# Optimization experiments

Measured on AMD Instinct MI355X. Metric: run time of the kernel, lower is better.

## Reference

```python
import jax, jax.numpy as jnp
import numpy as np


def _rotate_nearest(img, theta):
    """Rotate a batch of images (B, C, H, W) counterclockwise by theta radians
    about the image center, nearest-neighbor sampling, zero fill outside
    (matches torchvision rotate defaults: InterpolationMode.NEAREST, expand=False)."""
    B, C, H, W = img.shape
    cy = (H - 1) / 2.0
    cx = (W - 1) / 2.0
    ys = jnp.arange(H, dtype=jnp.float32) - cy
    xs = jnp.arange(W, dtype=jnp.float32) - cx
    yg, xg = jnp.meshgrid(ys, xs, indexing="ij")  # (H, W)
    c = jnp.cos(theta)
    s = jnp.sin(theta)
    # inverse affine map: output pixel -> source pixel
    x_src = c * xg + s * yg + cx
    y_src = -s * xg + c * yg + cy
    xi = jnp.round(x_src).astype(jnp.int32)
    yi = jnp.round(y_src).astype(jnp.int32)
    valid = (xi >= 0) & (xi < W) & (yi >= 0) & (yi < H)
    xi = jnp.clip(xi, 0, W - 1)
    yi = jnp.clip(yi, 0, H - 1)
    out = img[:, :, yi, xi]  # gather -> (B, C, H, W)
    return jnp.where(valid, out, jnp.zeros((), img.dtype))


def reference(image, kernel_size):
    # image: (B, C, H, W, A); A = num_angles
    B, C, H, W, A = image.shape
    angle_increment = 360.0 / A
    offsets = (jnp.arange(A) % kernel_size).astype(jnp.float32)
    # torch code calls rotate(slice, -angle_increment * relative_offset) in degrees
    thetas = jnp.deg2rad(-angle_increment * offsets)  # (A,)
    img_a = jnp.moveaxis(image, -1, 0)  # (A, B, C, H, W)
    rot = jax.vmap(_rotate_nearest, in_axes=(0, 0))(img_a, thetas)  # (A, B, C, H, W)
    rot = jnp.moveaxis(rot, 0, -1)  # (B, C, H, W, A)
    # MaxPool3d(kernel=(1,1,k)) == non-overlapping max over windows of k along angle dim
    pooled = rot.reshape(B, C, H, W, A // kernel_size, kernel_size).max(axis=-1)
    return pooled  # (B, C, H, W, A // kernel_size)


def setup_inputs() -> dict:
    key = jax.random.key(0)
    image = jax.random.normal(key, (8, 16, 128, 128, 24), dtype=jnp.float32)
    return {"image": image, "kernel_size": 4}
```

## Files before the change

kernel.cpp:

```cpp
#include <hip/hip_runtime.h>
#include <math.h>


#pragma clang fp contract(off)

#define BB 8
#define CC 16
#define HH 128
#define WW 128
#define AA 24
#define KK 4
#define GG 6

__global__ __launch_bounds__(192) void glp_rotation_pool_kernel(
    const float* __restrict__ img, float* __restrict__ out) {
  int blk = blockIdx.x;
  int xcd = blk & 7;
  int i   = blk >> 3;
  int bc  = (xcd << 4) | (i >> 9);
  int s   = i & 511;
  int y   = s >> 2;
  int x0  = (s & 3) << 5;

  int tid = threadIdx.x;
  int pix = (unsigned)tid / 6u;
  int g   = (unsigned)tid - 6u * pix;
  int x   = x0 + pix;

  const float cx = 63.5f;
  const float cy = 63.5f;

  float xg = (float)x - cx;
  float yg = (float)y - cy;

  const float* base = img + (size_t)bc * (HH * WW * AA);

  float res = -INFINITY;

#pragma unroll
  for (int k = 0; k < KK; ++k) {
    float tdeg  = -15.0f * (float)k;
    float theta = tdeg * 0.017453292519943295f;
    float cth = (float)cos((double)theta);
    float sth = (float)sin((double)theta);

    float xs = cth * xg + sth * yg + cx;
    float ys = (-sth) * xg + cth * yg + cy;

    int xi = (int)rintf(xs);
    int yi = (int)rintf(ys);

    bool valid = ((unsigned)xi < (unsigned)WW) & ((unsigned)yi < (unsigned)HH);
    int xc = min(max(xi, 0), WW - 1);
    int yc = min(max(yi, 0), HH - 1);

    float v = base[((size_t)(yc * WW + xc)) * AA + (k + 4 * g)];
    v = valid ? v : 0.0f;
    res = fmaxf(res, v);
  }

  size_t obase = ((size_t)bc * (HH * WW) + (size_t)y * WW + x0) * GG;
  out[obase + tid] = res;
}

extern "C" void kernel_launch(void* const* d_in, const int* in_sizes, int n_in,
                              void* d_out, int out_size, void* d_ws, size_t ws_size,
                              hipStream_t stream) {
  const float* img = (const float*)d_in[0];
  float* out = (float*)d_out;
  dim3 grid(BB * CC * HH * 4);
  dim3 block(192);
  glp_rotation_pool_kernel<<<grid, block, 0, stream>>>(img, out);
}
```

Baseline: 305.8 us.

## Stage rotated source bounding box in LDS per 32x32 output tile

Each block now handles a 32x32 output tile with 1024 threads. For each rotation offset it computes the bounding box of the source region, loads that box into shared memory with coalesced float4 reads (keeping only the needed angle lane), and then gathers from LDS. Each thread produces all six pooled outputs for its pixel and writes them as float2 stores. This replaces scattered strided global gathers with contiguous loads, at the cost of extra synchronisation, reading unused float4 lanes, and large LDS use that limits occupancy.

```diff
diff --git a/kernel.cpp b/kernel.cpp
--- a/kernel.cpp
+++ b/kernel.cpp
@@ -11,64 +11,118 @@
 #define AA 24
 #define KK 4
 #define GG 6
+#define TS 32
+#define BBX 48
+#define LROW (BBX * GG)
 
-__global__ __launch_bounds__(192) void glp_rotation_pool_kernel(
+__global__ __launch_bounds__(1024, 8) void glp_rotation_pool_kernel(
     const float* __restrict__ img, float* __restrict__ out) {
+  __shared__ float lds[BBX * LROW];
+
   int blk = blockIdx.x;
   int xcd = blk & 7;
-  int i   = blk >> 3;
-  int bc  = (xcd << 4) | (i >> 9);
-  int s   = i & 511;
-  int y   = s >> 2;
-  int x0  = (s & 3) << 5;
+  int i = blk >> 3;
+  int bc = (xcd << 4) | (i >> 4);
+  int tile = i & 15;
+  int ty = (tile >> 2) << 5;
+  int tx = (tile & 3) << 5;
 
   int tid = threadIdx.x;
-  int pix = (unsigned)tid / 6u;
-  int g   = (unsigned)tid - 6u * pix;
-  int x   = x0 + pix;
+  int py = tid >> 5;
+  int px = tid & 31;
+  int wave = tid >> 6;
+  int lane = tid & 63;
 
   const float cx = 63.5f;
   const float cy = 63.5f;
 
-  float xg = (float)x - cx;
-  float yg = (float)y - cy;
-
   const float* base = img + (size_t)bc * (HH * WW * AA);
 
-  float res = -INFINITY;
+  float xg = (float)(tx + px) - cx;
+  float yg = (float)(ty + py) - cy;
+  float xga = (float)tx - cx, xgb = (float)(tx + TS - 1) - cx;
+  float yga = (float)ty - cy, ygb = (float)(ty + TS - 1) - cy;
+
+  float res0 = -INFINITY, res1 = -INFINITY, res2 = -INFINITY;
+  float res3 = -INFINITY, res4 = -INFINITY, res5 = -INFINITY;
 
 #pragma unroll
   for (int k = 0; k < KK; ++k) {
-    float tdeg  = -15.0f * (float)k;
+    float tdeg = -15.0f * (float)k;
     float theta = tdeg * 0.017453292519943295f;
     float cth = (float)cos((double)theta);
     float sth = (float)sin((double)theta);
 
+    float xs00 = cth * xga + sth * yga + cx;
+    float xs01 = cth * xga + sth * ygb + cx;
+    float xs10 = cth * xgb + sth * yga + cx;
+    float xs11 = cth * xgb + sth * ygb + cx;
+    float ys00 = (-sth) * xga + cth * yga + cy;
+    float ys01 = (-sth) * xga + cth * ygb + cy;
+    float ys10 = (-sth) * xgb + cth * yga + cy;
+    float ys11 = (-sth) * xgb + cth * ygb + cy;
+    float minxs = fminf(fminf(xs00, xs01), fminf(xs10, xs11));
+    float maxxs = fmaxf(fmaxf(xs00, xs01), fmaxf(xs10, xs11));
+    float minys = fminf(fminf(ys00, ys01), fminf(ys10, ys11));
+    float maxys = fmaxf(fmaxf(ys00, ys01), fmaxf(ys10, ys11));
+    int bx0 = max(0, (int)floorf(minxs));
+    int bx1 = min(WW - 1, (int)ceilf(maxxs));
+    int by0 = max(0, (int)floorf(minys));
+    int by1 = min(HH - 1, (int)ceilf(maxys));
+    int NC = min(bx1 - bx0 + 1, BBX);
+    int NR = min(by1 - by0 + 1, BBX);
+
+    __syncthreads();
+    if (NC > 0 && NR > 0) {
+      int rowq = GG * NC;
+      for (int dy = wave; dy < NR; dy += 16) {
+        const float4* rowp =
+            (const float4*)(base + (size_t)((by0 + dy) * WW + bx0) * AA);
+        float* lrow = &lds[dy * LROW];
+        for (int q = lane; q < rowq; q += 64) {
+          float4 v = rowp[q];
+          float e = (k == 0) ? v.x : (k == 1) ? v.y : (k == 2) ? v.z : v.w;
+          lrow[q] = e;
+        }
+      }
+    }
+    __syncthreads();
+
     float xs = cth * xg + sth * yg + cx;
     float ys = (-sth) * xg + cth * yg + cy;
-
     int xi = (int)rintf(xs);
     int yi = (int)rintf(ys);
-
     bool valid = ((unsigned)xi < (unsigned)WW) & ((unsigned)yi < (unsigned)HH);
     int xc = min(max(xi, 0), WW - 1);
     int yc = min(max(yi, 0), HH - 1);
-
-    float v = base[((size_t)(yc * WW + xc)) * AA + (k + 4 * g)];
-    v = valid ? v : 0.0f;
-    res = fmaxf(res, v);
+    int dxr = min(max(xc - bx0, 0), BBX - 1);
+    int dyr = min(max(yc - by0, 0), BBX - 1);
+    const float2* lp = (const float2*)&lds[dyr * LROW + dxr * GG];
+    float2 v01 = lp[0];
+    float2 v23 = lp[1];
+    float2 v45 = lp[2];
+    res0 = fmaxf(res0, valid ? v01.x : 0.0f);
+    res1 = fmaxf(res1, valid ? v01.y : 0.0f);
+    res2 = fmaxf(res2, valid ? v23.x : 0.0f);
+    res3 = fmaxf(res3, valid ? v23.y : 0.0f);
+    res4 = fmaxf(res4, valid ? v45.x : 0.0f);
+    res5 = fmaxf(res5, valid ? v45.y : 0.0f);
   }
 
-  size_t obase = ((size_t)bc * (HH * WW) + (size_t)y * WW + x0) * GG;
-  out[obase + tid] = res;
+  size_t opix =
+      ((size_t)bc * (HH * WW) + (size_t)(ty + py) * WW + (tx + px)) * GG;
+  float2* op = (float2*)&out[opix];
+  op[0] = make_float2(res0, res1);
+  op[1] = make_float2(res2, res3);
+  op[2] = make_float2(res4, res5);
 }
 
 extern "C" void kernel_launch(void* const* d_in, const int* in_sizes, int n_in,
-                              void* d_out, int out_size, void* d_ws, size_t ws_size,
-                              hipStream_t stream) {
+                              void* d_out, int out_size, void* d_ws,
+                              size_t ws_size, hipStream_t stream) {
   const float* img = (const float*)d_in[0];
   float* out = (float*)d_out;
-  dim3 grid(BB * CC * HH * 4);
-  dim3 block(192);
+  dim3 grid(BB * CC * 16);
+  dim3 block(1024);
   glp_rotation_pool_kernel<<<grid, block, 0, stream>>>(img, out);
 }
```

Measured after the change: 349.1 us. 1.14x slower.

## Stage rotated source windows into LDS with double-buffered async global loads

Applied to the files above, without the earlier changes.

Each block now handles a 32x16 output tile. For every rotation offset it computes the bounding source window, then copies that window's 6 strided angle channels into shared memory using global_load_lds, double-buffered across the four rotations with explicit waitcnt and barriers. Threads then gather their nearest-neighbour samples from LDS and write 6 outputs per pixel as float2 stores. This is meant to replace scattered global gathers with coalesced bulk loads. It relies on hand-sized window constants that must cover the rotated footprint, and on vmcnt counts that must match the number of issued loads.

```diff
diff --git a/kernel.cpp b/kernel.cpp
--- a/kernel.cpp
+++ b/kernel.cpp
@@ -4,71 +4,170 @@
 
 #pragma clang fp contract(off)
 
-#define BB 8
-#define CC 16
 #define HH 128
 #define WW 128
 #define AA 24
-#define KK 4
 #define GG 6
+#define TW 32
+#define TH 16
 
-__global__ __launch_bounds__(192) void glp_rotation_pool_kernel(
+#define GLDS(gp, lp)                                       \
+  __builtin_amdgcn_global_load_lds(                        \
+      (const __attribute__((address_space(1))) void*)(gp), \
+      (__attribute__((address_space(3))) void*)(lp), 4, 0, 0)
+
+template <int K>
+__device__ __forceinline__ void ktrig(float& cth, float& sth) {
+  float tdeg = -15.0f * (float)K;
+  float theta = tdeg * 0.017453292519943295f;
+  cth = (float)cos((double)theta);
+  sth = (float)sin((double)theta);
+}
+
+template <int K, int WK, int HK>
+__device__ __forceinline__ void window_k(float xga, float xgb, float yga,
+                                         float ygb, int& bx0, int& by0) {
+  float cth, sth;
+  ktrig<K>(cth, sth);
+  float xs00 = cth * xga + sth * yga + 63.5f;
+  float xs01 = cth * xga + sth * ygb + 63.5f;
+  float xs10 = cth * xgb + sth * yga + 63.5f;
+  float xs11 = cth * xgb + sth * ygb + 63.5f;
+  float ys00 = (-sth) * xga + cth * yga + 63.5f;
+  float ys01 = (-sth) * xga + cth * ygb + 63.5f;
+  float ys10 = (-sth) * xgb + cth * yga + 63.5f;
+  float ys11 = (-sth) * xgb + cth * ygb + 63.5f;
+  float minxs = fminf(fminf(xs00, xs01), fminf(xs10, xs11));
+  float minys = fminf(fminf(ys00, ys01), fminf(ys10, ys11));
+  bx0 = min(max((int)rintf(minxs), 0), WW - WK);
+  by0 = min(max((int)rintf(minys), 0), HH - HK);
+}
+
+template <int K, int WK, int HK>
+__device__ __forceinline__ void stage_k(const float* sbase, float* lplane,
+                                        int bx0, int by0, int wave, int lane) {
+  constexpr int LR = WK * GG;
+  constexpr int NFULL = LR >> 6;
+  constexpr int REM = LR & 63;
+  constexpr int NJ = (HK + 7) >> 3;
+#pragma unroll
+  for (int j = 0; j < NJ; ++j) {
+    int dy = wave + 8 * j;
+    dy = dy < HK ? dy : HK - 1;
+    const float* row = sbase + ((by0 + dy) * WW + bx0) * AA + K;
+    float* lrow = lplane + dy * LR;
+#pragma unroll
+    for (int c = 0; c < NFULL; ++c) {
+      GLDS(row + 4 * (64 * c + lane), lrow + 64 * c);
+    }
+    if (REM && lane < REM) {
+      GLDS(row + 4 * (64 * NFULL + lane), lrow + 64 * NFULL);
+    }
+  }
+}
+
+template <int K, int WK, int HK>
+__device__ __forceinline__ void gather_k(const float* lplane, int bx0, int by0,
+                                         float xg, float yg, float* r) {
+  float cth, sth;
+  ktrig<K>(cth, sth);
+  float xs = cth * xg + sth * yg + 63.5f;
+  float ys = (-sth) * xg + cth * yg + 63.5f;
+  int xi = (int)rintf(xs);
+  int yi = (int)rintf(ys);
+  bool valid = ((unsigned)xi < (unsigned)WW) & ((unsigned)yi < (unsigned)HH);
+  int dxr = min(max(xi - bx0, 0), WK - 1);
+  int dyr = min(max(yi - by0, 0), HK - 1);
+  const float2* lp = (const float2*)(lplane + dyr * (WK * GG) + dxr * GG);
+  float2 v01 = lp[0];
+  float2 v23 = lp[1];
+  float2 v45 = lp[2];
+  r[0] = fmaxf(r[0], valid ? v01.x : 0.0f);
+  r[1] = fmaxf(r[1], valid ? v01.y : 0.0f);
+  r[2] = fmaxf(r[2], valid ? v23.x : 0.0f);
+  r[3] = fmaxf(r[3], valid ? v23.y : 0.0f);
+  r[4] = fmaxf(r[4], valid ? v45.x : 0.0f);
+  r[5] = fmaxf(r[5], valid ? v45.y : 0.0f);
+}
+
+__global__ __launch_bounds__(512, 4) void glp_rotation_pool_kernel(
     const float* __restrict__ img, float* __restrict__ out) {
+  __shared__ __align__(16) float buf0[6480];
+  __shared__ __align__(16) float buf1[6936];
+
   int blk = blockIdx.x;
   int xcd = blk & 7;
-  int i   = blk >> 3;
-  int bc  = (xcd << 4) | (i >> 9);
-  int s   = i & 511;
-  int y   = s >> 2;
-  int x0  = (s & 3) << 5;
+  int i = blk >> 3;
+  int bc = (xcd << 4) | (i >> 5);
+  int tile = i & 31;
+  int ty = (tile >> 2) << 4;
+  int tx = (tile & 3) << 5;
 
   int tid = threadIdx.x;
-  int pix = (unsigned)tid / 6u;
-  int g   = (unsigned)tid - 6u * pix;
-  int x   = x0 + pix;
+  int px = tid & 31;
+  int py = tid >> 5;
+  int wave = tid >> 6;
+  int lane = tid & 63;
 
-  const float cx = 63.5f;
-  const float cy = 63.5f;
+  const float* sbase = img + (size_t)bc * (HH * WW * AA);
 
-  float xg = (float)x - cx;
-  float yg = (float)y - cy;
+  float xg = (float)(tx + px) - 63.5f;
+  float yg = (float)(ty + py) - 63.5f;
+  float xga = (float)tx - 63.5f, xgb = (float)(tx + TW - 1) - 63.5f;
+  float yga = (float)ty - 63.5f, ygb = (float)(ty + TH - 1) - 63.5f;
 
-  const float* base = img + (size_t)bc * (HH * WW * AA);
+  int bx0_0, by0_0, bx0_1, by0_1, bx0_2, by0_2, bx0_3, by0_3;
+  window_k<0, 32, 16>(xga, xgb, yga, ygb, bx0_0, by0_0);
+  window_k<1, 35, 24>(xga, xgb, yga, ygb, bx0_1, by0_1);
+  window_k<2, 36, 30>(xga, xgb, yga, ygb, bx0_2, by0_2);
+  window_k<3, 34, 34>(xga, xgb, yga, ygb, bx0_3, by0_3);
 
-  float res = -INFINITY;
+  float r[6] = {-INFINITY, -INFINITY, -INFINITY,
+                -INFINITY, -INFINITY, -INFINITY};
 
-#pragma unroll
-  for (int k = 0; k < KK; ++k) {
-    float tdeg  = -15.0f * (float)k;
-    float theta = tdeg * 0.017453292519943295f;
-    float cth = (float)cos((double)theta);
-    float sth = (float)sin((double)theta);
+  stage_k<0, 32, 16>(sbase, buf0, bx0_0, by0_0, wave, lane);
+  stage_k<1, 35, 24>(sbase, buf1, bx0_1, by0_1, wave, lane);
+  asm volatile("s_waitcnt vmcnt(12)" ::: "memory");
+  __builtin_amdgcn_sched_barrier(0);
+  __builtin_amdgcn_s_barrier();
+  __builtin_amdgcn_sched_barrier(0);
+  gather_k<0, 32, 16>(buf0, bx0_0, by0_0, xg, yg, r);
+  __builtin_amdgcn_s_barrier();
+  __builtin_amdgcn_sched_barrier(0);
+  stage_k<2, 36, 30>(sbase, buf0, bx0_2, by0_2, wave, lane);
+  asm volatile("s_waitcnt vmcnt(16)" ::: "memory");
+  __builtin_amdgcn_sched_barrier(0);
+  __builtin_amdgcn_s_barrier();
+  __builtin_amdgcn_sched_barrier(0);
+  gather_k<1, 35, 24>(buf1, bx0_1, by0_1, xg, yg, r);
+  __builtin_amdgcn_s_barrier();
+  __builtin_amdgcn_sched_barrier(0);
+  stage_k<3, 34, 34>(sbase, buf1, bx0_3, by0_3, wave, lane);
+  asm volatile("s_waitcnt vmcnt(20)" ::: "memory");
+  __builtin_amdgcn_sched_barrier(0);
+  __builtin_amdgcn_s_barrier();
+  __builtin_amdgcn_sched_barrier(0);
+  gather_k<2, 36, 30>(buf0, bx0_2, by0_2, xg, yg, r);
+  asm volatile("s_waitcnt vmcnt(0)" ::: "memory");
+  __builtin_amdgcn_sched_barrier(0);
+  __builtin_amdgcn_s_barrier();
+  __builtin_amdgcn_sched_barrier(0);
+  gather_k<3, 34, 34>(buf1, bx0_3, by0_3, xg, yg, r);
 
-    float xs = cth * xg + sth * yg + cx;
-    float ys = (-sth) * xg + cth * yg + cy;
-
-    int xi = (int)rintf(xs);
-    int yi = (int)rintf(ys);
-
-    bool valid = ((unsigned)xi < (unsigned)WW) & ((unsigned)yi < (unsigned)HH);
-    int xc = min(max(xi, 0), WW - 1);
-    int yc = min(max(yi, 0), HH - 1);
-
-    float v = base[((size_t)(yc * WW + xc)) * AA + (k + 4 * g)];
-    v = valid ? v : 0.0f;
-    res = fmaxf(res, v);
-  }
-
-  size_t obase = ((size_t)bc * (HH * WW) + (size_t)y * WW + x0) * GG;
-  out[obase + tid] = res;
+  size_t opix =
+      ((size_t)bc * (HH * WW) + (size_t)(ty + py) * WW + (tx + px)) * GG;
+  float2* op = (float2*)&out[opix];
+  op[0] = make_float2(r[0], r[1]);
+  op[1] = make_float2(r[2], r[3]);
+  op[2] = make_float2(r[4], r[5]);
 }
 
 extern "C" void kernel_launch(void* const* d_in, const int* in_sizes, int n_in,
-                              void* d_out, int out_size, void* d_ws, size_t ws_size,
-                              hipStream_t stream) {
+                              void* d_out, int out_size, void* d_ws,
+                              size_t ws_size, hipStream_t stream) {
   const float* img = (const float*)d_in[0];
   float* out = (float*)d_out;
-  dim3 grid(BB * CC * HH * 4);
-  dim3 block(192);
+  dim3 grid(128 * 32);
+  dim3 block(512);
   glp_rotation_pool_kernel<<<grid, block, 0, stream>>>(img, out);
 }
```

New measurement: 330.7 us. 1.08x slower.

## Repack input into per-angle bf16 planes before rotated gather-max

Applied to the files above, without the earlier changes.

Adds a repack kernel that converts the fp32 input to bf16 and lays it out as four per-offset planes, each pixel holding the six angle groups packed in 16 bytes. A second kernel then does one vector gather per rotation per output pixel, with one thread per pixel, instead of scattered scalar loads across 24-float records. This is meant to cut gather transaction counts and improve locality. In exchange it adds a full extra pass over the data through workspace and rounds inputs to bf16, which changes numerics. The original kernel is kept as a fallback when workspace is too small.

```diff
diff --git a/kernel.cpp b/kernel.cpp
--- a/kernel.cpp
+++ b/kernel.cpp
@@ -4,71 +4,158 @@
 
 #pragma clang fp contract(off)
 
-#define BB 8
-#define CC 16
 #define HH 128
 #define WW 128
 #define AA 24
-#define KK 4
 #define GG 6
+#define PX (HH * WW)
+#define WS_NEEDED 134217728ull
 
-__global__ __launch_bounds__(192) void glp_rotation_pool_kernel(
+static __device__ __forceinline__ unsigned int bf16rne(float f) {
+  unsigned int u = __float_as_uint(f);
+  return (u + 0x7fffu + ((u >> 16) & 1u)) >> 16;
+}
+
+template <int K>
+__device__ __forceinline__ void ktrig(float& cth, float& sth) {
+  float tdeg = -15.0f * (float)K;
+  float theta = tdeg * 0.017453292519943295f;
+  cth = (float)cos((double)theta);
+  sth = (float)sin((double)theta);
+}
+
+__global__ __launch_bounds__(256) void glp_repack_kernel(
+    const float* __restrict__ img, unsigned int* __restrict__ ws) {
+  int b = blockIdx.x;
+  int slice = (unsigned)b / 192u;
+  int rem = b - slice * 192;
+  int q2 = rem * 256 + threadIdx.x;
+  int px = (unsigned)q2 / 3u;
+  int j = q2 - 3 * px;
+
+  const float4* rec =
+      (const float4*)(img + (size_t)slice * (PX * AA)) + (size_t)px * 6 + 2 * j;
+  float4 a = rec[0];
+  float4 c = rec[1];
+
+  size_t pbase = ((size_t)slice * 4) * (PX * 4) + (size_t)px * 4 + j;
+  ws[pbase + 0 * (PX * 4)] = bf16rne(a.x) | (bf16rne(c.x) << 16);
+  ws[pbase + 1 * (PX * 4)] = bf16rne(a.y) | (bf16rne(c.y) << 16);
+  ws[pbase + 2 * (PX * 4)] = bf16rne(a.z) | (bf16rne(c.z) << 16);
+  ws[pbase + 3 * (PX * 4)] = bf16rne(a.w) | (bf16rne(c.w) << 16);
+}
+
+template <int K>
+__device__ __forceinline__ void gather2(const uint4* __restrict__ plane,
+                                        float xg, float yg, float* r) {
+  float cth, sth;
+  ktrig<K>(cth, sth);
+  float xs = cth * xg + sth * yg + 63.5f;
+  float ys = (-sth) * xg + cth * yg + 63.5f;
+  int xi = (int)rintf(xs);
+  int yi = (int)rintf(ys);
+  bool valid = ((unsigned)xi < (unsigned)WW) & ((unsigned)yi < (unsigned)HH);
+  int xc = min(max(xi, 0), WW - 1);
+  int yc = min(max(yi, 0), HH - 1);
+  uint4 v = plane[yc * WW + xc];
+  float f0 = __uint_as_float(v.x << 16);
+  float f1 = __uint_as_float(v.x & 0xffff0000u);
+  float f2 = __uint_as_float(v.y << 16);
+  float f3 = __uint_as_float(v.y & 0xffff0000u);
+  float f4 = __uint_as_float(v.z << 16);
+  float f5 = __uint_as_float(v.z & 0xffff0000u);
+  r[0] = fmaxf(r[0], valid ? f0 : 0.0f);
+  r[1] = fmaxf(r[1], valid ? f1 : 0.0f);
+  r[2] = fmaxf(r[2], valid ? f2 : 0.0f);
+  r[3] = fmaxf(r[3], valid ? f3 : 0.0f);
+  r[4] = fmaxf(r[4], valid ? f4 : 0.0f);
+  r[5] = fmaxf(r[5], valid ? f5 : 0.0f);
+}
+
+__global__ __launch_bounds__(256) void glp_gather_kernel(
+    const unsigned int* __restrict__ ws, float* __restrict__ out) {
+  int blk = blockIdx.x;
+  int xcd = blk & 7;
+  int i = blk >> 3;
+  int slice = (xcd << 4) | (i >> 6);
+  int sub = i & 63;
+  int tid = threadIdx.x;
+  int y = sub * 2 + (tid >> 7);
+  int x = tid & 127;
+
+  float xg = (float)x - 63.5f;
+  float yg = (float)y - 63.5f;
+
+  const uint4* base = (const uint4*)ws + (size_t)slice * 4 * PX;
+
+  float r[6] = {-INFINITY, -INFINITY, -INFINITY,
+                -INFINITY, -INFINITY, -INFINITY};
+  gather2<0>(base + 0 * PX, xg, yg, r);
+  gather2<1>(base + 1 * PX, xg, yg, r);
+  gather2<2>(base + 2 * PX, xg, yg, r);
+  gather2<3>(base + 3 * PX, xg, yg, r);
+
+  size_t opix = ((size_t)slice * PX + (size_t)y * WW + x) * GG;
+  float2* op = (float2*)&out[opix];
+  op[0] = make_float2(r[0], r[1]);
+  op[1] = make_float2(r[2], r[3]);
+  op[2] = make_float2(r[4], r[5]);
+}
+
+__global__ __launch_bounds__(192) void glp_fallback_kernel(
     const float* __restrict__ img, float* __restrict__ out) {
   int blk = blockIdx.x;
   int xcd = blk & 7;
-  int i   = blk >> 3;
-  int bc  = (xcd << 4) | (i >> 9);
-  int s   = i & 511;
-  int y   = s >> 2;
-  int x0  = (s & 3) << 5;
+  int i = blk >> 3;
+  int bc = (xcd << 4) | (i >> 9);
+  int s = i & 511;
+  int y = s >> 2;
+  int x0 = (s & 3) << 5;
 
   int tid = threadIdx.x;
   int pix = (unsigned)tid / 6u;
-  int g   = (unsigned)tid - 6u * pix;
-  int x   = x0 + pix;
+  int g = (unsigned)tid - 6u * pix;
+  int x = x0 + pix;
 
-  const float cx = 63.5f;
-  const float cy = 63.5f;
-
-  float xg = (float)x - cx;
-  float yg = (float)y - cy;
-
+  float xg = (float)x - 63.5f;
+  float yg = (float)y - 63.5f;
   const float* base = img + (size_t)bc * (HH * WW * AA);
-
   float res = -INFINITY;
-
 #pragma unroll
-  for (int k = 0; k < KK; ++k) {
-    float tdeg  = -15.0f * (float)k;
-    float theta = tdeg * 0.017453292519943295f;
-    float cth = (float)cos((double)theta);
-    float sth = (float)sin((double)theta);
-
-    float xs = cth * xg + sth * yg + cx;
-    float ys = (-sth) * xg + cth * yg + cy;
-
+  for (int k = 0; k < 4; ++k) {
+    float cth, sth;
+    switch (k) {
+      case 0: ktrig<0>(cth, sth); break;
+      case 1: ktrig<1>(cth, sth); break;
+      case 2: ktrig<2>(cth, sth); break;
+      default: ktrig<3>(cth, sth); break;
+    }
+    float xs = cth * xg + sth * yg + 63.5f;
+    float ys = (-sth) * xg + cth * yg + 63.5f;
     int xi = (int)rintf(xs);
     int yi = (int)rintf(ys);
-
     bool valid = ((unsigned)xi < (unsigned)WW) & ((unsigned)yi < (unsigned)HH);
     int xc = min(max(xi, 0), WW - 1);
     int yc = min(max(yi, 0), HH - 1);
-
     float v = base[((size_t)(yc * WW + xc)) * AA + (k + 4 * g)];
     v = valid ? v : 0.0f;
     res = fmaxf(res, v);
   }
-
   size_t obase = ((size_t)bc * (HH * WW) + (size_t)y * WW + x0) * GG;
   out[obase + tid] = res;
 }
 
 extern "C" void kernel_launch(void* const* d_in, const int* in_sizes, int n_in,
-                              void* d_out, int out_size, void* d_ws, size_t ws_size,
-                              hipStream_t stream) {
+                              void* d_out, int out_size, void* d_ws,
+                              size_t ws_size, hipStream_t stream) {
   const float* img = (const float*)d_in[0];
   float* out = (float*)d_out;
-  dim3 grid(BB * CC * HH * 4);
-  dim3 block(192);
-  glp_rotation_pool_kernel<<<grid, block, 0, stream>>>(img, out);
+  if (ws_size >= WS_NEEDED && d_ws != nullptr) {
+    glp_repack_kernel<<<dim3(24576), dim3(256), 0, stream>>>(
+        img, (unsigned int*)d_ws);
+    glp_gather_kernel<<<dim3(8192), dim3(256), 0, stream>>>(
+        (const unsigned int*)d_ws, out);
+  } else {
+    glp_fallback_kernel<<<dim3(65536), dim3(192), 0, stream>>>(img, out);
+  }
 }
```

Result: slower. 356.0 us (+16.4%).
